# Kernel optimization log

Measured on AMD Instinct MI355X. Metric: run time of the kernel, lower is better.

The kernel has to match this reference:

```python
import jax, jax.numpy as jnp
import numpy as np

SEQ, BS, H, I, E = 2048, 4, 2048, 4096, 8


def setup_inputs() -> dict:
    key = jax.random.key(0)
    ks = jax.random.split(key, 5)
    s = 0.02
    return {
        "hidden_states": jax.random.normal(ks[0], (SEQ, BS, H), dtype=jnp.float32),
        "router_w": jax.random.normal(ks[1], (H, E), dtype=jnp.float32) * s,
        "gate_w": jax.random.normal(ks[2], (E, H, I), dtype=jnp.float32) * s,
        "up_w": jax.random.normal(ks[3], (E, H, I), dtype=jnp.float32) * s,
        "down_w": jax.random.normal(ks[4], (E, I, H), dtype=jnp.float32) * s,
    }


def reference(hidden_states, router_w, gate_w, up_w, down_w):
    # Router: [S,B,H] @ [H,E] -> [S,B,E]; top-1 routing (num_experts_per_tok == 1)
    router_logits = jnp.einsum("sbh,he->sbe", hidden_states, router_w)
    routing_indices = jnp.argmax(router_logits, axis=-1)  # [S,B]
    # sigmoid routing weights are computed but NOT applied in the original combine
    routing_weights = jax.nn.sigmoid(jnp.max(router_logits, axis=-1))  # noqa: F841

    out = jnp.zeros_like(hidden_states)
    for e in range(E):  # small fixed expert count
        mask = (routing_indices == e)[..., None]  # [S,B,1]
        g = jnp.einsum("sbh,hi->sbi", hidden_states, gate_w[e])
        u = jnp.einsum("sbh,hi->sbi", hidden_states, up_w[e])
        y = jnp.einsum("sbi,ih->sbh", jax.nn.silu(g) * u, down_w[e])
        out = out + jnp.where(mask, y, jnp.zeros((), out.dtype))
    return out
```

## Files before the change

### kernel.cpp

```cpp
#include <hip/hip_runtime.h>
#include <hip/hip_bf16.h>

#define T_TOKENS 8192
#define H_DIM 2048
#define I_DIM 4096
#define E_EXP 8
#define PAD_ROWS 9216

typedef __bf16 bf16x8 __attribute__((ext_vector_type(8)));
typedef float floatx4 __attribute__((ext_vector_type(4)));
typedef unsigned short ushort8 __attribute__((ext_vector_type(8)));

__device__ __forceinline__ unsigned short f2bf(float f) {
  union { float f; unsigned int i; } c; c.f = f;
  unsigned int x = c.i;
  unsigned int r = x + 0x7fffu + ((x >> 16) & 1u);
  return (unsigned short)(r >> 16);
}

__device__ __forceinline__ float bf2float(unsigned short u) {
  union { unsigned int i; float f; } c; c.i = ((unsigned int)u) << 16;
  return c.f;
}

__device__ __forceinline__ void gload_lds16(const void* g, void* l) {
  __builtin_amdgcn_global_load_lds(
      (const __attribute__((address_space(1))) void*)g,
      (__attribute__((address_space(3))) void*)l, 16, 0, 0);
}

__global__ __launch_bounds__(256) void xcvt_kernel(const float* __restrict__ x,
                                                   unsigned short* __restrict__ xb,
                                                   int* __restrict__ hdr) {
  if (blockIdx.x == 0 && threadIdx.x < 32) hdr[threadIdx.x] = 0;
  int i = (blockIdx.x * 256 + threadIdx.x) * 4;
  floatx4 v = *(const floatx4*)(x + i);
  unsigned short o0 = f2bf(v[0]), o1 = f2bf(v[1]), o2 = f2bf(v[2]), o3 = f2bf(v[3]);
  ushort4 o; o.x = o0; o.y = o1; o.z = o2; o.w = o3;
  *(ushort4*)(xb + i) = o;
}

__global__ __launch_bounds__(256) void router_kernel(const float* __restrict__ x,
                                                     const float* __restrict__ rw,
                                                     int* __restrict__ idx,
                                                     int* __restrict__ hdr) {
  int lane = threadIdx.x & 63;
  int t = blockIdx.x * 4 + (threadIdx.x >> 6);
  const float* xr = x + (size_t)t * H_DIM;
  float acc[8];
#pragma unroll
  for (int e = 0; e < 8; ++e) acc[e] = 0.f;
  for (int i = lane; i < H_DIM; i += 64) {
    float h = xr[i];
    floatx4 r0 = *(const floatx4*)(rw + i * 8);
    floatx4 r1 = *(const floatx4*)(rw + i * 8 + 4);
#pragma unroll
    for (int e = 0; e < 4; ++e) { acc[e] += h * r0[e]; acc[e + 4] += h * r1[e]; }
  }
#pragma unroll
  for (int off = 32; off > 0; off >>= 1)
#pragma unroll
    for (int e = 0; e < 8; ++e) acc[e] += __shfl_xor(acc[e], off, 64);
  if (lane == 0) {
    int best = 0; float bv = acc[0];
#pragma unroll
    for (int e = 1; e < 8; ++e) if (acc[e] > bv) { bv = acc[e]; best = e; }
    idx[t] = best;
    atomicAdd(&hdr[best], 1);
  }
}

__global__ __launch_bounds__(256) void setup_kernel(int* __restrict__ hdr,
                                                    int* __restrict__ rows) {
  if (threadIdx.x == 0) {
    int b = 0;
    for (int e = 0; e < 8; ++e) {
      hdr[16 + e] = b;
      b += ((hdr[e] + 127) >> 7) << 7;
    }
  }
  for (int i = threadIdx.x; i < PAD_ROWS; i += 256) rows[i] = -1;
}

__global__ __launch_bounds__(256) void scatter_kernel(const int* __restrict__ idx,
                                                      int* __restrict__ hdr,
                                                      int* __restrict__ rows) {
  int t = blockIdx.x * 256 + threadIdx.x;
  int e = idx[t];
  int p = atomicAdd(&hdr[8 + e], 1);
  rows[hdr[16 + e] + p] = t;
}

template <int K, int N>
__global__ __launch_bounds__(256) void cvt_tile_kernel(const float* __restrict__ W,
                                                       unsigned short* __restrict__ Wt) {
  const int e = blockIdx.z;
  const int kg = blockIdx.y;
  const int nb = blockIdx.x * 1024;
  const int n0 = threadIdx.x * 4;
  const float* src = W + (size_t)e * K * N + (size_t)kg * 8 * N + nb + n0;
  unsigned short* dst = Wt + (size_t)e * K * N
                        + ((size_t)kg * (N / 16) + (nb >> 4)) * 128;
  floatx4 a[8];
#pragma unroll
  for (int kk = 0; kk < 8; ++kk) a[kk] = *(const floatx4*)(src + (size_t)kk * N);
#pragma unroll
  for (int nn = 0; nn < 4; ++nn) {
    const int n = n0 + nn;
    ushort8 o;
#pragma unroll
    for (int kk = 0; kk < 8; ++kk) o[kk] = f2bf(a[kk][nn]);
    *(ushort8*)(dst + (size_t)(n >> 4) * 128 + (n & 15) * 8) = o;
  }
}

__global__ __launch_bounds__(256, 2) void moe_gemm_gu(
    const unsigned short* __restrict__ A,
    const unsigned short* __restrict__ Bg,
    const unsigned short* __restrict__ Bu,
    const int* __restrict__ hdr,
    const int* __restrict__ rows,
    unsigned short* __restrict__ inter) {
  const int e = blockIdx.z;
  const int cnt = hdr[e];
  if ((int)blockIdx.y * 128 >= cnt) return;
  const int seg = hdr[16 + e];

  const int tid = threadIdx.x;
  const int lane = tid & 63;
  const int wv = tid >> 6;
  const int wm = (wv & 1) * 64;
  const int wn = (wv >> 1) * 64;
  const int q = lane >> 4;
  const int l15 = lane & 15;

  __shared__ unsigned short sA[128 * 64];
  __shared__ unsigned short sBg[64 * 128];
  __shared__ unsigned short sBu[64 * 128];

  const int lr = lane >> 3;
  const int colsw = (lane & 7) ^ lr;
  const unsigned short* aptr[4];
#pragma unroll
  for (int j = 0; j < 4; ++j) {
    const int R = j * 32 + wv * 8 + lr;
    int ar = rows[seg + blockIdx.y * 128 + R];
    if (ar < 0) ar = 0;
    aptr[j] = A + (size_t)ar * H_DIM + colsw * 8;
  }

  const int N16 = I_DIM / 16;
  const int ng0 = blockIdx.x * 8;
  const unsigned short* BgE = Bg + (size_t)e * I_DIM * H_DIM;
  const unsigned short* BuE = Bu + (size_t)e * I_DIM * H_DIM;

  floatx4 accg[4][4], accu[4][4];
#pragma unroll
  for (int a = 0; a < 4; ++a)
#pragma unroll
    for (int b = 0; b < 4; ++b) {
      accg[a][b] = (floatx4){0.f, 0.f, 0.f, 0.f};
      accu[a][b] = (floatx4){0.f, 0.f, 0.f, 0.f};
    }

  const int ubB = q * 1024 + l15 * 8;
  const int wn16o = (wn >> 4) * 128;

  for (int kt = 0; kt < H_DIM; kt += 64) {
#pragma unroll
    for (int j = 0; j < 4; ++j) {
      gload_lds16(aptr[j] + kt, sA + (j * 32 + wv * 8) * 64);
      const int g = j * 4 + wv;
      const int kgg = (kt >> 3) + (g >> 1);
      const size_t so = (size_t)(kgg * N16 + ng0 + (g & 1) * 4) * 128 + lane * 8;
      gload_lds16(BgE + so, sBg + g * 512);
      gload_lds16(BuE + so, sBu + g * 512);
    }
    __syncthreads();
#pragma unroll
    for (int ks = 0; ks < 64; ks += 32) {
      const int sbase = ks >> 3;
      const int bbase = ks * 128 + wn16o + ubB;
      bf16x8 af[4], bfr[4];
#pragma unroll
      for (int fm = 0; fm < 4; ++fm) {
        const int ra = wm + fm * 16 + l15;
        af[fm] = __builtin_bit_cast(bf16x8,
            *(const ushort8*)(sA + ra * 64 + (((q + sbase) ^ (ra & 7)) << 3)));
      }
#pragma unroll
      for (int fn = 0; fn < 4; ++fn)
        bfr[fn] = __builtin_bit_cast(bf16x8,
            *(const ushort8*)(sBg + bbase + fn * 128));
#pragma unroll
      for (int fm = 0; fm < 4; ++fm)
#pragma unroll
        for (int fn = 0; fn < 4; ++fn)
          accg[fm][fn] = __builtin_amdgcn_mfma_f32_16x16x32_bf16(af[fm], bfr[fn],
                                                                 accg[fm][fn], 0, 0, 0);
#pragma unroll
      for (int fn = 0; fn < 4; ++fn)
        bfr[fn] = __builtin_bit_cast(bf16x8,
            *(const ushort8*)(sBu + bbase + fn * 128));
#pragma unroll
      for (int fm = 0; fm < 4; ++fm)
#pragma unroll
        for (int fn = 0; fn < 4; ++fn)
          accu[fm][fn] = __builtin_amdgcn_mfma_f32_16x16x32_bf16(af[fm], bfr[fn],
                                                                 accu[fm][fn], 0, 0, 0);
    }
    __syncthreads();
  }

#pragma unroll
  for (int fm = 0; fm < 4; ++fm)
#pragma unroll
    for (int fn = 0; fn < 4; ++fn)
#pragma unroll
      for (int rr = 0; rr < 4; ++rr) {
        const int row = wm + fm * 16 + q * 4 + rr;
        const int col = wn + fn * 16 + l15;
        const int gm = blockIdx.y * 128 + row;
        const int gn = blockIdx.x * 128 + col;
        const float g = accg[fm][fn][rr];
        const float u = accu[fm][fn][rr];
        const float s = g / (1.f + __expf(-g));
        inter[(size_t)(seg + gm) * I_DIM + gn] = f2bf(s * u);
      }
}

__global__ __launch_bounds__(256, 2) void moe_gemm_down(
    const unsigned short* __restrict__ A,
    const unsigned short* __restrict__ Bt,
    const int* __restrict__ hdr,
    const int* __restrict__ rows,
    float* __restrict__ outp) {
  const int e = blockIdx.z;
  const int cnt = hdr[e];
  if ((int)blockIdx.y * 128 >= cnt) return;
  const int seg = hdr[16 + e];

  const int tid = threadIdx.x;
  const int lane = tid & 63;
  const int wv = tid >> 6;
  const int wm = (wv & 1) * 64;
  const int wn = (wv >> 1) * 64;
  const int q = lane >> 4;
  const int l15 = lane & 15;

  __shared__ unsigned short sA[128 * 64];
  __shared__ unsigned short sB0[64 * 128];
  __shared__ unsigned short sB1[64 * 128];

  const int lr = lane >> 3;
  const int colsw = (lane & 7) ^ lr;
  const unsigned short* aptr[4];
#pragma unroll
  for (int j = 0; j < 4; ++j) {
    const int R = j * 32 + wv * 8 + lr;
    aptr[j] = A + (size_t)(seg + blockIdx.y * 128 + R) * I_DIM + colsw * 8;
  }

  const int N16 = H_DIM / 16;
  const int ng0 = blockIdx.x * 16;
  const unsigned short* Be = Bt + (size_t)e * H_DIM * I_DIM;

  floatx4 acc0[4][4], acc1[4][4];
#pragma unroll
  for (int a = 0; a < 4; ++a)
#pragma unroll
    for (int b = 0; b < 4; ++b) {
      acc0[a][b] = (floatx4){0.f, 0.f, 0.f, 0.f};
      acc1[a][b] = (floatx4){0.f, 0.f, 0.f, 0.f};
    }

  const int ubB = q * 1024 + l15 * 8;
  const int wn16o = (wn >> 4) * 128;

  for (int kt = 0; kt < I_DIM; kt += 64) {
#pragma unroll
    for (int j = 0; j < 4; ++j) {
      gload_lds16(aptr[j] + kt, sA + (j * 32 + wv * 8) * 64);
      const int g = j * 4 + wv;
      const int kgg = (kt >> 3) + (g >> 1);
      const size_t so0 = (size_t)(kgg * N16 + ng0 + (g & 1) * 4) * 128 + lane * 8;
      const size_t so1 = (size_t)(kgg * N16 + ng0 + 8 + (g & 1) * 4) * 128 + lane * 8;
      gload_lds16(Be + so0, sB0 + g * 512);
      gload_lds16(Be + so1, sB1 + g * 512);
    }
    __syncthreads();
#pragma unroll
    for (int ks = 0; ks < 64; ks += 32) {
      const int sbase = ks >> 3;
      const int bbase = ks * 128 + wn16o + ubB;
      bf16x8 af[4], bfr[4];
#pragma unroll
      for (int fm = 0; fm < 4; ++fm) {
        const int ra = wm + fm * 16 + l15;
        af[fm] = __builtin_bit_cast(bf16x8,
            *(const ushort8*)(sA + ra * 64 + (((q + sbase) ^ (ra & 7)) << 3)));
      }
#pragma unroll
      for (int fn = 0; fn < 4; ++fn)
        bfr[fn] = __builtin_bit_cast(bf16x8,
            *(const ushort8*)(sB0 + bbase + fn * 128));
#pragma unroll
      for (int fm = 0; fm < 4; ++fm)
#pragma unroll
        for (int fn = 0; fn < 4; ++fn)
          acc0[fm][fn] = __builtin_amdgcn_mfma_f32_16x16x32_bf16(af[fm], bfr[fn],
                                                                 acc0[fm][fn], 0, 0, 0);
#pragma unroll
      for (int fn = 0; fn < 4; ++fn)
        bfr[fn] = __builtin_bit_cast(bf16x8,
            *(const ushort8*)(sB1 + bbase + fn * 128));
#pragma unroll
      for (int fm = 0; fm < 4; ++fm)
#pragma unroll
        for (int fn = 0; fn < 4; ++fn)
          acc1[fm][fn] = __builtin_amdgcn_mfma_f32_16x16x32_bf16(af[fm], bfr[fn],
                                                                 acc1[fm][fn], 0, 0, 0);
    }
    __syncthreads();
  }

#pragma unroll
  for (int fm = 0; fm < 4; ++fm)
#pragma unroll
    for (int rr = 0; rr < 4; ++rr) {
      const int row = wm + fm * 16 + q * 4 + rr;
      const int tok = rows[seg + blockIdx.y * 128 + row];
      if (tok < 0) continue;
      float* orow = outp + (size_t)tok * H_DIM + blockIdx.x * 256;
#pragma unroll
      for (int fn = 0; fn < 4; ++fn) {
        const int col = wn + fn * 16 + l15;
        orow[col]       = acc0[fm][fn][rr];
        orow[128 + col] = acc1[fm][fn][rr];
      }
    }
}

extern "C" void kernel_launch(void* const* d_in, const int* in_sizes, int n_in,
                              void* d_out, int out_size, void* d_ws, size_t ws_size,
                              hipStream_t stream) {
  const float* hidden   = (const float*)d_in[0];
  const float* router_w = (const float*)d_in[1];
  const float* gate_w   = (const float*)d_in[2];
  const float* up_w     = (const float*)d_in[3];
  const float* down_w   = (const float*)d_in[4];
  float* out = (float*)d_out;

  char* ws = (char*)d_ws;
  int* hdr  = (int*)ws;
  int* idx  = (int*)(ws + 1024);
  int* rows = (int*)(ws + 33792);
  unsigned short* x_bf  = (unsigned short*)(ws + 70656);
  unsigned short* inter = (unsigned short*)(ws + 33625088);
  unsigned short* W1    = (unsigned short*)(ws + 109122560);
  unsigned short* W2    = (unsigned short*)(ws + 243340288);
  unsigned short* downt = W1;

  xcvt_kernel<<<T_TOKENS * H_DIM / 1024, 256, 0, stream>>>(hidden, x_bf, hdr);
  router_kernel<<<T_TOKENS / 4, 256, 0, stream>>>(hidden, router_w, idx, hdr);
  setup_kernel<<<1, 256, 0, stream>>>(hdr, rows);
  scatter_kernel<<<T_TOKENS / 256, 256, 0, stream>>>(idx, hdr, rows);

  cvt_tile_kernel<H_DIM, I_DIM><<<dim3(I_DIM / 1024, H_DIM / 8, E_EXP), 256, 0, stream>>>(gate_w, W1);
  cvt_tile_kernel<H_DIM, I_DIM><<<dim3(I_DIM / 1024, H_DIM / 8, E_EXP), 256, 0, stream>>>(up_w, W2);

  moe_gemm_gu<<<dim3(I_DIM / 128, 64, E_EXP), 256, 0, stream>>>(
      x_bf, W1, W2, hdr, rows, inter);

  cvt_tile_kernel<I_DIM, H_DIM><<<dim3(H_DIM / 1024, I_DIM / 8, E_EXP), 256, 0, stream>>>(down_w, downt);
  moe_gemm_down<<<dim3(H_DIM / 256, 64, E_EXP), 256, 0, stream>>>(
      inter, downt, hdr, rows, out);
}
```

Measured before the change: 1.508 ms.

## Fuse weight conversion into router and gate/up GEMM launches

Merges the x conversion, the router, and the gate/up weight bf16 conversion into one launch, with extra blocks doing the weight tiling. The down-weight conversion is folded into the gate/up GEMM grid as extra y-blocks writing to a separate workspace buffer, used only when the workspace is large enough. Weight reads become nontemporal loads and the header is zeroed with a memset. This cuts launch count and lets conversion overlap with GEMM blocks, at the cost of more workspace and mixed-role blocks in the GEMM launch.

```diff
diff --git a/kernel.cpp b/kernel.cpp
--- a/kernel.cpp
+++ b/kernel.cpp
@@ -29,33 +29,66 @@
       (__attribute__((address_space(3))) void*)l, 16, 0, 0);
 }
 
-__global__ __launch_bounds__(256) void xcvt_kernel(const float* __restrict__ x,
-                                                   unsigned short* __restrict__ xb,
-                                                   int* __restrict__ hdr) {
-  if (blockIdx.x == 0 && threadIdx.x < 32) hdr[threadIdx.x] = 0;
-  int i = (blockIdx.x * 256 + threadIdx.x) * 4;
-  floatx4 v = *(const floatx4*)(x + i);
-  unsigned short o0 = f2bf(v[0]), o1 = f2bf(v[1]), o2 = f2bf(v[2]), o3 = f2bf(v[3]);
-  ushort4 o; o.x = o0; o.y = o1; o.z = o2; o.w = o3;
-  *(ushort4*)(xb + i) = o;
-}
-
-__global__ __launch_bounds__(256) void router_kernel(const float* __restrict__ x,
-                                                     const float* __restrict__ rw,
-                                                     int* __restrict__ idx,
-                                                     int* __restrict__ hdr) {
-  int lane = threadIdx.x & 63;
-  int t = blockIdx.x * 4 + (threadIdx.x >> 6);
+__device__ __forceinline__ void cvt_slab(const float* __restrict__ W,
+                                         unsigned short* __restrict__ Wt,
+                                         int K, int N, int e, int kg, int nb,
+                                         int tid) {
+  const int n0 = tid * 4;
+  const float* src = W + (size_t)e * K * N + (size_t)kg * 8 * N + nb + n0;
+  unsigned short* dst = Wt + (size_t)e * K * N
+                        + ((size_t)kg * (N >> 4) + (nb >> 4)) * 128;
+  floatx4 a[8];
+#pragma unroll
+  for (int kk = 0; kk < 8; ++kk)
+    a[kk] = __builtin_nontemporal_load((const floatx4*)(src + (size_t)kk * N));
+#pragma unroll
+  for (int nn = 0; nn < 4; ++nn) {
+    const int n = n0 + nn;
+    ushort8 o;
+#pragma unroll
+    for (int kk = 0; kk < 8; ++kk) o[kk] = f2bf(a[kk][nn]);
+    *(ushort8*)(dst + (size_t)(n >> 4) * 128 + (n & 15) * 8) = o;
+  }
+}
+
+__global__ __launch_bounds__(256) void router_cvt_kernel(
+    const float* __restrict__ x, const float* __restrict__ rw,
+    const float* __restrict__ gw, const float* __restrict__ uw,
+    unsigned short* __restrict__ xb, int* __restrict__ idx,
+    int* __restrict__ hdr, unsigned short* __restrict__ Wg,
+    unsigned short* __restrict__ Wu) {
+  if (blockIdx.x >= 2048) {
+    int bid = blockIdx.x - 2048;
+    const float* W = (bid < 8192) ? gw : uw;
+    unsigned short* Wt = (bid < 8192) ? Wg : Wu;
+    bid &= 8191;
+    const int e = bid >> 10;
+    const int rem = bid & 1023;
+    cvt_slab(W, Wt, H_DIM, I_DIM, e, rem >> 2, (rem & 3) * 1024, threadIdx.x);
+    return;
+  }
+  const int lane = threadIdx.x & 63;
+  const int t = blockIdx.x * 4 + (threadIdx.x >> 6);
   const float* xr = x + (size_t)t * H_DIM;
+  unsigned short* xbr = xb + (size_t)t * H_DIM;
   float acc[8];
 #pragma unroll
   for (int e = 0; e < 8; ++e) acc[e] = 0.f;
-  for (int i = lane; i < H_DIM; i += 64) {
-    float h = xr[i];
-    floatx4 r0 = *(const floatx4*)(rw + i * 8);
-    floatx4 r1 = *(const floatx4*)(rw + i * 8 + 4);
-#pragma unroll
-    for (int e = 0; e < 4; ++e) { acc[e] += h * r0[e]; acc[e + 4] += h * r1[e]; }
+#pragma unroll
+  for (int j = 0; j < 8; ++j) {
+    const int c0 = (lane + j * 64) * 4;
+    floatx4 v = *(const floatx4*)(xr + c0);
+    ushort4 o;
+    o.x = f2bf(v[0]); o.y = f2bf(v[1]); o.z = f2bf(v[2]); o.w = f2bf(v[3]);
+    *(ushort4*)(xbr + c0) = o;
+#pragma unroll
+    for (int cc = 0; cc < 4; ++cc) {
+      const float h = v[cc];
+      floatx4 r0 = *(const floatx4*)(rw + (size_t)(c0 + cc) * 8);
+      floatx4 r1 = *(const floatx4*)(rw + (size_t)(c0 + cc) * 8 + 4);
+#pragma unroll
+      for (int e = 0; e < 4; ++e) { acc[e] += h * r0[e]; acc[e + 4] += h * r1[e]; }
+    }
   }
 #pragma unroll
   for (int off = 32; off > 0; off >>= 1)
@@ -91,27 +124,12 @@
   rows[hdr[16 + e] + p] = t;
 }
 
-template <int K, int N>
-__global__ __launch_bounds__(256) void cvt_tile_kernel(const float* __restrict__ W,
+__global__ __launch_bounds__(256) void cvt_down_kernel(const float* __restrict__ W,
                                                        unsigned short* __restrict__ Wt) {
-  const int e = blockIdx.z;
-  const int kg = blockIdx.y;
-  const int nb = blockIdx.x * 1024;
-  const int n0 = threadIdx.x * 4;
-  const float* src = W + (size_t)e * K * N + (size_t)kg * 8 * N + nb + n0;
-  unsigned short* dst = Wt + (size_t)e * K * N
-                        + ((size_t)kg * (N / 16) + (nb >> 4)) * 128;
-  floatx4 a[8];
-#pragma unroll
-  for (int kk = 0; kk < 8; ++kk) a[kk] = *(const floatx4*)(src + (size_t)kk * N);
-#pragma unroll
-  for (int nn = 0; nn < 4; ++nn) {
-    const int n = n0 + nn;
-    ushort8 o;
-#pragma unroll
-    for (int kk = 0; kk < 8; ++kk) o[kk] = f2bf(a[kk][nn]);
-    *(ushort8*)(dst + (size_t)(n >> 4) * 128 + (n & 15) * 8) = o;
-  }
+  const int bid = blockIdx.x;
+  const int e = bid >> 10;
+  const int rem = bid & 1023;
+  cvt_slab(W, Wt, I_DIM, H_DIM, e, rem >> 1, (rem & 1) * 1024, threadIdx.x);
 }
 
 __global__ __launch_bounds__(256, 2) void moe_gemm_gu(
@@ -120,7 +138,16 @@
     const unsigned short* __restrict__ Bu,
     const int* __restrict__ hdr,
     const int* __restrict__ rows,
-    unsigned short* __restrict__ inter) {
+    unsigned short* __restrict__ inter,
+    const float* __restrict__ dw,
+    unsigned short* __restrict__ Wd) {
+  if (blockIdx.y >= 64) {
+    const int cid = (((int)blockIdx.y - 64) * 32 + (int)blockIdx.x) * 8 + (int)blockIdx.z;
+    const int e = cid >> 10;
+    const int rem = cid & 1023;
+    cvt_slab(dw, Wd, I_DIM, H_DIM, e, rem >> 1, (rem & 1) * 1024, threadIdx.x);
+    return;
+  }
   const int e = blockIdx.z;
   const int cnt = hdr[e];
   if ((int)blockIdx.y * 128 >= cnt) return;
@@ -359,20 +386,25 @@
   unsigned short* inter = (unsigned short*)(ws + 33625088);
   unsigned short* W1    = (unsigned short*)(ws + 109122560);
   unsigned short* W2    = (unsigned short*)(ws + 243340288);
-  unsigned short* downt = W1;
-
-  xcvt_kernel<<<T_TOKENS * H_DIM / 1024, 256, 0, stream>>>(hidden, x_bf, hdr);
-  router_kernel<<<T_TOKENS / 4, 256, 0, stream>>>(hidden, router_w, idx, hdr);
+  unsigned short* W3    = (unsigned short*)(ws + 377558016);
+  const bool big = ws_size >= 511775744ull;
+
+  hipMemsetAsync(hdr, 0, 128, stream);
+  router_cvt_kernel<<<2048 + 16384, 256, 0, stream>>>(
+      hidden, router_w, gate_w, up_w, x_bf, idx, hdr, W1, W2);
   setup_kernel<<<1, 256, 0, stream>>>(hdr, rows);
   scatter_kernel<<<T_TOKENS / 256, 256, 0, stream>>>(idx, hdr, rows);
 
-  cvt_tile_kernel<H_DIM, I_DIM><<<dim3(I_DIM / 1024, H_DIM / 8, E_EXP), 256, 0, stream>>>(gate_w, W1);
-  cvt_tile_kernel<H_DIM, I_DIM><<<dim3(I_DIM / 1024, H_DIM / 8, E_EXP), 256, 0, stream>>>(up_w, W2);
-
-  moe_gemm_gu<<<dim3(I_DIM / 128, 64, E_EXP), 256, 0, stream>>>(
-      x_bf, W1, W2, hdr, rows, inter);
-
-  cvt_tile_kernel<I_DIM, H_DIM><<<dim3(H_DIM / 1024, I_DIM / 8, E_EXP), 256, 0, stream>>>(down_w, downt);
-  moe_gemm_down<<<dim3(H_DIM / 256, 64, E_EXP), 256, 0, stream>>>(
-      inter, downt, hdr, rows, out);
-}
+  if (big) {
+    moe_gemm_gu<<<dim3(I_DIM / 128, 96, E_EXP), 256, 0, stream>>>(
+        x_bf, W1, W2, hdr, rows, inter, down_w, W3);
+    moe_gemm_down<<<dim3(H_DIM / 256, 64, E_EXP), 256, 0, stream>>>(
+        inter, W3, hdr, rows, out);
+  } else {
+    moe_gemm_gu<<<dim3(I_DIM / 128, 64, E_EXP), 256, 0, stream>>>(
+        x_bf, W1, W2, hdr, rows, inter, nullptr, nullptr);
+    cvt_down_kernel<<<8192, 256, 0, stream>>>(down_w, W1);
+    moe_gemm_down<<<dim3(H_DIM / 256, 64, E_EXP), 256, 0, stream>>>(
+        inter, W1, hdr, rows, out);
+  }
+}
```

New measurement: 1.447 ms. 4.0% less time.

## Fuse fp32-to-bf16 weight conversion into MoE GEMM tile loads and merge x conversion into router

Applied to the files above, without the earlier changes.

Removes the separate weight conversion kernels that rewrote all gate, up and down weights to bf16 in a tiled layout. The GEMMs now read fp32 weights directly, convert them to bf16 in registers and store them into padded LDS tiles. The activation conversion is folded into the router kernel, and the header is zeroed with a memset. This drops a full extra pass over roughly 800MB of weights, but each GEMM tile block now re-reads and re-converts fp32 weights for every M tile. It also replaces the asynchronous direct-to-LDS weight loads with synchronous register loads, which means twice the global bytes per weight read and less overlap.

```diff
diff --git a/kernel.cpp b/kernel.cpp
--- a/kernel.cpp
+++ b/kernel.cpp
@@ -18,44 +18,39 @@
   return (unsigned short)(r >> 16);
 }
 
-__device__ __forceinline__ float bf2float(unsigned short u) {
-  union { unsigned int i; float f; } c; c.i = ((unsigned int)u) << 16;
-  return c.f;
-}
-
 __device__ __forceinline__ void gload_lds16(const void* g, void* l) {
   __builtin_amdgcn_global_load_lds(
       (const __attribute__((address_space(1))) void*)g,
       (__attribute__((address_space(3))) void*)l, 16, 0, 0);
 }
 
-__global__ __launch_bounds__(256) void xcvt_kernel(const float* __restrict__ x,
-                                                   unsigned short* __restrict__ xb,
-                                                   int* __restrict__ hdr) {
-  if (blockIdx.x == 0 && threadIdx.x < 32) hdr[threadIdx.x] = 0;
-  int i = (blockIdx.x * 256 + threadIdx.x) * 4;
-  floatx4 v = *(const floatx4*)(x + i);
-  unsigned short o0 = f2bf(v[0]), o1 = f2bf(v[1]), o2 = f2bf(v[2]), o3 = f2bf(v[3]);
-  ushort4 o; o.x = o0; o.y = o1; o.z = o2; o.w = o3;
-  *(ushort4*)(xb + i) = o;
-}
-
 __global__ __launch_bounds__(256) void router_kernel(const float* __restrict__ x,
                                                      const float* __restrict__ rw,
+                                                     unsigned short* __restrict__ xb,
                                                      int* __restrict__ idx,
                                                      int* __restrict__ hdr) {
-  int lane = threadIdx.x & 63;
-  int t = blockIdx.x * 4 + (threadIdx.x >> 6);
+  const int lane = threadIdx.x & 63;
+  const int t = blockIdx.x * 4 + (threadIdx.x >> 6);
   const float* xr = x + (size_t)t * H_DIM;
+  unsigned short* xbr = xb + (size_t)t * H_DIM;
   float acc[8];
 #pragma unroll
   for (int e = 0; e < 8; ++e) acc[e] = 0.f;
-  for (int i = lane; i < H_DIM; i += 64) {
-    float h = xr[i];
-    floatx4 r0 = *(const floatx4*)(rw + i * 8);
-    floatx4 r1 = *(const floatx4*)(rw + i * 8 + 4);
-#pragma unroll
-    for (int e = 0; e < 4; ++e) { acc[e] += h * r0[e]; acc[e + 4] += h * r1[e]; }
+#pragma unroll
+  for (int j = 0; j < 8; ++j) {
+    const int c0 = (lane + j * 64) * 4;
+    floatx4 v = *(const floatx4*)(xr + c0);
+    ushort4 o;
+    o.x = f2bf(v[0]); o.y = f2bf(v[1]); o.z = f2bf(v[2]); o.w = f2bf(v[3]);
+    *(ushort4*)(xbr + c0) = o;
+#pragma unroll
+    for (int cc = 0; cc < 4; ++cc) {
+      const float h = v[cc];
+      floatx4 r0 = *(const floatx4*)(rw + (size_t)(c0 + cc) * 8);
+      floatx4 r1 = *(const floatx4*)(rw + (size_t)(c0 + cc) * 8 + 4);
+#pragma unroll
+      for (int e = 0; e < 4; ++e) { acc[e] += h * r0[e]; acc[e + 4] += h * r1[e]; }
+    }
   }
 #pragma unroll
   for (int off = 32; off > 0; off >>= 1)
@@ -91,33 +86,10 @@
   rows[hdr[16 + e] + p] = t;
 }
 
-template <int K, int N>
-__global__ __launch_bounds__(256) void cvt_tile_kernel(const float* __restrict__ W,
-                                                       unsigned short* __restrict__ Wt) {
-  const int e = blockIdx.z;
-  const int kg = blockIdx.y;
-  const int nb = blockIdx.x * 1024;
-  const int n0 = threadIdx.x * 4;
-  const float* src = W + (size_t)e * K * N + (size_t)kg * 8 * N + nb + n0;
-  unsigned short* dst = Wt + (size_t)e * K * N
-                        + ((size_t)kg * (N / 16) + (nb >> 4)) * 128;
-  floatx4 a[8];
-#pragma unroll
-  for (int kk = 0; kk < 8; ++kk) a[kk] = *(const floatx4*)(src + (size_t)kk * N);
-#pragma unroll
-  for (int nn = 0; nn < 4; ++nn) {
-    const int n = n0 + nn;
-    ushort8 o;
-#pragma unroll
-    for (int kk = 0; kk < 8; ++kk) o[kk] = f2bf(a[kk][nn]);
-    *(ushort8*)(dst + (size_t)(n >> 4) * 128 + (n & 15) * 8) = o;
-  }
-}
-
 __global__ __launch_bounds__(256, 2) void moe_gemm_gu(
     const unsigned short* __restrict__ A,
-    const unsigned short* __restrict__ Bg,
-    const unsigned short* __restrict__ Bu,
+    const float* __restrict__ Bg,
+    const float* __restrict__ Bu,
     const int* __restrict__ hdr,
     const int* __restrict__ rows,
     unsigned short* __restrict__ inter) {
@@ -135,8 +107,8 @@
   const int l15 = lane & 15;
 
   __shared__ unsigned short sA[128 * 64];
-  __shared__ unsigned short sBg[64 * 128];
-  __shared__ unsigned short sBu[64 * 128];
+  __shared__ unsigned short sBg[128 * 72];
+  __shared__ unsigned short sBu[128 * 72];
 
   const int lr = lane >> 3;
   const int colsw = (lane & 7) ^ lr;
@@ -149,10 +121,10 @@
     aptr[j] = A + (size_t)ar * H_DIM + colsw * 8;
   }
 
-  const int N16 = I_DIM / 16;
-  const int ng0 = blockIdx.x * 8;
-  const unsigned short* BgE = Bg + (size_t)e * I_DIM * H_DIM;
-  const unsigned short* BuE = Bu + (size_t)e * I_DIM * H_DIM;
+  const int n4 = (tid & 31) * 4;
+  const int kb = (tid >> 5) * 8;
+  const float* BgE = Bg + (size_t)e * H_DIM * I_DIM;
+  const float* BuE = Bu + (size_t)e * H_DIM * I_DIM;
 
   floatx4 accg[4][4], accu[4][4];
 #pragma unroll
@@ -163,24 +135,37 @@
       accu[a][b] = (floatx4){0.f, 0.f, 0.f, 0.f};
     }
 
-  const int ubB = q * 1024 + l15 * 8;
-  const int wn16o = (wn >> 4) * 128;
-
   for (int kt = 0; kt < H_DIM; kt += 64) {
 #pragma unroll
-    for (int j = 0; j < 4; ++j) {
+    for (int j = 0; j < 4; ++j)
       gload_lds16(aptr[j] + kt, sA + (j * 32 + wv * 8) * 64);
-      const int g = j * 4 + wv;
-      const int kgg = (kt >> 3) + (g >> 1);
-      const size_t so = (size_t)(kgg * N16 + ng0 + (g & 1) * 4) * 128 + lane * 8;
-      gload_lds16(BgE + so, sBg + g * 512);
-      gload_lds16(BuE + so, sBu + g * 512);
+    {
+      const float* bp = BgE + (size_t)(kt + kb) * I_DIM + blockIdx.x * 128 + n4;
+      floatx4 r[8];
+#pragma unroll
+      for (int jj = 0; jj < 8; ++jj) r[jj] = *(const floatx4*)(bp + (size_t)jj * I_DIM);
+#pragma unroll
+      for (int i = 0; i < 4; ++i) {
+        ushort8 p;
+#pragma unroll
+        for (int jj = 0; jj < 8; ++jj) p[jj] = f2bf(r[jj][i]);
+        *(ushort8*)(sBg + (n4 + i) * 72 + kb) = p;
+      }
+      const float* bq = BuE + (size_t)(kt + kb) * I_DIM + blockIdx.x * 128 + n4;
+#pragma unroll
+      for (int jj = 0; jj < 8; ++jj) r[jj] = *(const floatx4*)(bq + (size_t)jj * I_DIM);
+#pragma unroll
+      for (int i = 0; i < 4; ++i) {
+        ushort8 p;
+#pragma unroll
+        for (int jj = 0; jj < 8; ++jj) p[jj] = f2bf(r[jj][i]);
+        *(ushort8*)(sBu + (n4 + i) * 72 + kb) = p;
+      }
     }
     __syncthreads();
 #pragma unroll
     for (int ks = 0; ks < 64; ks += 32) {
       const int sbase = ks >> 3;
-      const int bbase = ks * 128 + wn16o + ubB;
       bf16x8 af[4], bfr[4];
 #pragma unroll
       for (int fm = 0; fm < 4; ++fm) {
@@ -191,7 +176,7 @@
 #pragma unroll
       for (int fn = 0; fn < 4; ++fn)
         bfr[fn] = __builtin_bit_cast(bf16x8,
-            *(const ushort8*)(sBg + bbase + fn * 128));
+            *(const ushort8*)(sBg + (wn + fn * 16 + l15) * 72 + ks + q * 8));
 #pragma unroll
       for (int fm = 0; fm < 4; ++fm)
 #pragma unroll
@@ -201,7 +186,7 @@
 #pragma unroll
       for (int fn = 0; fn < 4; ++fn)
         bfr[fn] = __builtin_bit_cast(bf16x8,
-            *(const ushort8*)(sBu + bbase + fn * 128));
+            *(const ushort8*)(sBu + (wn + fn * 16 + l15) * 72 + ks + q * 8));
 #pragma unroll
       for (int fm = 0; fm < 4; ++fm)
 #pragma unroll
@@ -231,7 +216,7 @@
 
 __global__ __launch_bounds__(256, 2) void moe_gemm_down(
     const unsigned short* __restrict__ A,
-    const unsigned short* __restrict__ Bt,
+    const float* __restrict__ Bw,
     const int* __restrict__ hdr,
     const int* __restrict__ rows,
     float* __restrict__ outp) {
@@ -249,8 +234,8 @@
   const int l15 = lane & 15;
 
   __shared__ unsigned short sA[128 * 64];
-  __shared__ unsigned short sB0[64 * 128];
-  __shared__ unsigned short sB1[64 * 128];
+  __shared__ unsigned short sB0[128 * 72];
+  __shared__ unsigned short sB1[128 * 72];
 
   const int lr = lane >> 3;
   const int colsw = (lane & 7) ^ lr;
@@ -261,9 +246,9 @@
     aptr[j] = A + (size_t)(seg + blockIdx.y * 128 + R) * I_DIM + colsw * 8;
   }
 
-  const int N16 = H_DIM / 16;
-  const int ng0 = blockIdx.x * 16;
-  const unsigned short* Be = Bt + (size_t)e * H_DIM * I_DIM;
+  const int n4 = (tid & 31) * 4;
+  const int kb = (tid >> 5) * 8;
+  const float* Be = Bw + (size_t)e * I_DIM * H_DIM;
 
   floatx4 acc0[4][4], acc1[4][4];
 #pragma unroll
@@ -274,25 +259,37 @@
       acc1[a][b] = (floatx4){0.f, 0.f, 0.f, 0.f};
     }
 
-  const int ubB = q * 1024 + l15 * 8;
-  const int wn16o = (wn >> 4) * 128;
-
   for (int kt = 0; kt < I_DIM; kt += 64) {
 #pragma unroll
-    for (int j = 0; j < 4; ++j) {
+    for (int j = 0; j < 4; ++j)
       gload_lds16(aptr[j] + kt, sA + (j * 32 + wv * 8) * 64);
-      const int g = j * 4 + wv;
-      const int kgg = (kt >> 3) + (g >> 1);
-      const size_t so0 = (size_t)(kgg * N16 + ng0 + (g & 1) * 4) * 128 + lane * 8;
-      const size_t so1 = (size_t)(kgg * N16 + ng0 + 8 + (g & 1) * 4) * 128 + lane * 8;
-      gload_lds16(Be + so0, sB0 + g * 512);
-      gload_lds16(Be + so1, sB1 + g * 512);
+    {
+      const float* bp = Be + (size_t)(kt + kb) * H_DIM + blockIdx.x * 256 + n4;
+      floatx4 r[8];
+#pragma unroll
+      for (int jj = 0; jj < 8; ++jj) r[jj] = *(const floatx4*)(bp + (size_t)jj * H_DIM);
+#pragma unroll
+      for (int i = 0; i < 4; ++i) {
+        ushort8 p;
+#pragma unroll
+        for (int jj = 0; jj < 8; ++jj) p[jj] = f2bf(r[jj][i]);
+        *(ushort8*)(sB0 + (n4 + i) * 72 + kb) = p;
+      }
+      const float* bq = bp + 128;
+#pragma unroll
+      for (int jj = 0; jj < 8; ++jj) r[jj] = *(const floatx4*)(bq + (size_t)jj * H_DIM);
+#pragma unroll
+      for (int i = 0; i < 4; ++i) {
+        ushort8 p;
+#pragma unroll
+        for (int jj = 0; jj < 8; ++jj) p[jj] = f2bf(r[jj][i]);
+        *(ushort8*)(sB1 + (n4 + i) * 72 + kb) = p;
+      }
     }
     __syncthreads();
 #pragma unroll
     for (int ks = 0; ks < 64; ks += 32) {
       const int sbase = ks >> 3;
-      const int bbase = ks * 128 + wn16o + ubB;
       bf16x8 af[4], bfr[4];
 #pragma unroll
       for (int fm = 0; fm < 4; ++fm) {
@@ -303,7 +300,7 @@
 #pragma unroll
       for (int fn = 0; fn < 4; ++fn)
         bfr[fn] = __builtin_bit_cast(bf16x8,
-            *(const ushort8*)(sB0 + bbase + fn * 128));
+            *(const ushort8*)(sB0 + (wn + fn * 16 + l15) * 72 + ks + q * 8));
 #pragma unroll
       for (int fm = 0; fm < 4; ++fm)
 #pragma unroll
@@ -313,7 +310,7 @@
 #pragma unroll
       for (int fn = 0; fn < 4; ++fn)
         bfr[fn] = __builtin_bit_cast(bf16x8,
-            *(const ushort8*)(sB1 + bbase + fn * 128));
+            *(const ushort8*)(sB1 + (wn + fn * 16 + l15) * 72 + ks + q * 8));
 #pragma unroll
       for (int fm = 0; fm < 4; ++fm)
 #pragma unroll
@@ -357,22 +354,14 @@
   int* rows = (int*)(ws + 33792);
   unsigned short* x_bf  = (unsigned short*)(ws + 70656);
   unsigned short* inter = (unsigned short*)(ws + 33625088);
-  unsigned short* W1    = (unsigned short*)(ws + 109122560);
-  unsigned short* W2    = (unsigned short*)(ws + 243340288);
-  unsigned short* downt = W1;
-
-  xcvt_kernel<<<T_TOKENS * H_DIM / 1024, 256, 0, stream>>>(hidden, x_bf, hdr);
-  router_kernel<<<T_TOKENS / 4, 256, 0, stream>>>(hidden, router_w, idx, hdr);
+
+  hipMemsetAsync(hdr, 0, 128, stream);
+  router_kernel<<<T_TOKENS / 4, 256, 0, stream>>>(hidden, router_w, x_bf, idx, hdr);
   setup_kernel<<<1, 256, 0, stream>>>(hdr, rows);
   scatter_kernel<<<T_TOKENS / 256, 256, 0, stream>>>(idx, hdr, rows);
 
-  cvt_tile_kernel<H_DIM, I_DIM><<<dim3(I_DIM / 1024, H_DIM / 8, E_EXP), 256, 0, stream>>>(gate_w, W1);
-  cvt_tile_kernel<H_DIM, I_DIM><<<dim3(I_DIM / 1024, H_DIM / 8, E_EXP), 256, 0, stream>>>(up_w, W2);
-
   moe_gemm_gu<<<dim3(I_DIM / 128, 64, E_EXP), 256, 0, stream>>>(
-      x_bf, W1, W2, hdr, rows, inter);
-
-  cvt_tile_kernel<I_DIM, H_DIM><<<dim3(H_DIM / 1024, I_DIM / 8, E_EXP), 256, 0, stream>>>(down_w, downt);
+      x_bf, gate_w, up_w, hdr, rows, inter);
   moe_gemm_down<<<dim3(H_DIM / 256, 64, E_EXP), 256, 0, stream>>>(
-      inter, downt, hdr, rows, out);
-}
+      inter, down_w, hdr, rows, out);
+}
```

Measured after the change: 1.915 ms. 1.27x slower.
